# Performance work log

Measured on AMD Instinct MI355X. Metric: run time of the kernel, lower is better.

## Reference

```python
import jax, jax.numpy as jnp
import numpy as np

T_IN, T_TGT, B = 192, 192, 128
XDIM, CH, H, Z, OUT = 64, 2, 512, 128, 64
XIN = XDIM * CH


def _gru_cell(h, x_proj, Whh, bhh):
    # torch GRU gate order: r, z, n
    hp = h @ Whh.T + bhh
    xr, xz, xn = jnp.split(x_proj, 3, axis=-1)
    hr, hz, hn = jnp.split(hp, 3, axis=-1)
    r = jax.nn.sigmoid(xr + hr)
    zg = jax.nn.sigmoid(xz + hz)
    n = jnp.tanh(xn + r * hn)
    return (1.0 - zg) * n + zg * h


def _run_gru(xs, h0, Wih, bih, Whh, bhh):
    xp = xs @ Wih.T + bih  # [T, B, 3H] precomputed input projections
    def step(h, xpt):
        h2 = _gru_cell(h, xpt, Whh, bhh)
        return h2, h2
    hT, outs = jax.lax.scan(step, h0, xp)
    return outs, hT


def setup_inputs() -> dict:
    key = jax.random.key(0)
    ks = jax.random.split(key, 40)
    p = lambda i, shape: jax.random.normal(ks[i], shape, jnp.float32) * 0.05
    inp = {
        "x": jax.random.normal(ks[0], (T_IN, B, XIN), jnp.float32),
        "target": jax.random.normal(ks[1], (T_TGT, B, XDIM), jnp.float32),
        "eps_z": jax.random.normal(ks[2], (2, B, Z), jnp.float32),
        "eps_y": jax.random.normal(ks[3], (T_TGT, B, OUT), jnp.float32),
        # phi_x MLP
        "W_phi1": p(4, (H, XIN)), "b_phi1": jnp.zeros((H,), jnp.float32),
        "W_phi2": p(5, (H, H)), "b_phi2": jnp.zeros((H,), jnp.float32),
        # encoder bidirectional GRU
        "Wih_ef": p(6, (3 * H, H)), "bih_ef": jnp.zeros((3 * H,), jnp.float32),
        "Whh_ef": p(7, (3 * H, H)), "bhh_ef": jnp.zeros((3 * H,), jnp.float32),
        "Wih_eb": p(8, (3 * H, H)), "bih_eb": jnp.zeros((3 * H,), jnp.float32),
        "Whh_eb": p(9, (3 * H, H)), "bhh_eb": jnp.zeros((3 * H,), jnp.float32),
        # latent heads
        "W_mean": p(10, (Z, H)), "b_mean": jnp.zeros((Z,), jnp.float32),
        "W_std": p(11, (Z, H)), "b_std": jnp.zeros((Z,), jnp.float32),
        # first decoder hidden
        "W_fh": p(12, (H, 2 * Z)), "b_fh": jnp.zeros((H,), jnp.float32),
        # decoder GRU, input size H + 2Z (order: [z_expanded, state])
        "Wih_d": p(13, (3 * H, 2 * Z + H)), "bih_d": jnp.zeros((3 * H,), jnp.float32),
        "Whh_d": p(14, (3 * H, H)), "bhh_d": jnp.zeros((3 * H,), jnp.float32),
        # decoder output heads
        "W_dm": p(15, (OUT, H)), "b_dm": jnp.zeros((OUT,), jnp.float32),
        "W_ds": p(16, (OUT, H)), "b_ds": jnp.zeros((OUT,), jnp.float32),
        "epoch": 0,
    }
    return inp


def reference(x, target, eps_z, eps_y,
              W_phi1, b_phi1, W_phi2, b_phi2,
              Wih_ef, bih_ef, Whh_ef, bhh_ef,
              Wih_eb, bih_eb, Whh_eb, bhh_eb,
              W_mean, b_mean, W_std, b_std,
              W_fh, b_fh, Wih_d, bih_d, Whh_d, bhh_d,
              W_dm, b_dm, W_ds, b_ds, epoch):
    Bsz, h_dim = x.shape[1], W_phi1.shape[0]
    two_z = W_fh.shape[1]
    # phi_x
    phi = jax.nn.relu(jax.nn.relu(x @ W_phi1.T + b_phi1) @ W_phi2.T + b_phi2)
    h0 = jnp.zeros((Bsz, h_dim), phi.dtype)
    # bidirectional encoder: final hidden of each direction
    _, hf = _run_gru(phi, h0, Wih_ef, bih_ef, Whh_ef, bhh_ef)
    _, hb = _run_gru(phi[::-1], h0, Wih_eb, bih_eb, Whh_eb, bhh_eb)
    enc_h = jnp.stack([hf, hb])  # [2, B, H]
    latent_mean = enc_h @ W_mean.T + b_mean
    latent_std = jax.nn.softplus(enc_h @ W_std.T + b_std)
    z = eps_z * latent_std + latent_mean  # [2, B, Z]
    z_exp = jnp.concatenate([z[0], z[1]], axis=1)  # [B, 2Z]
    dec_h0 = jnp.tanh(z_exp @ W_fh.T + b_fh)
    # decoder input = concat([z_exp, state]); split Wih_d columns accordingly
    W_z, W_s = Wih_d[:, :two_z], Wih_d[:, two_z:]
    z_proj = z_exp @ W_z.T + bih_d  # constant part of input projection

    def step(carry, eps_t):
        h, s = carry  # s is previous decoder_out (zeros at t=0)
        xp = z_proj + s @ W_s.T
        h2 = _gru_cell(h, xp, Whh_d, bhh_d)
        m = jax.nn.softplus(h2 @ W_dm.T + b_dm)
        st = jax.nn.softplus(h2 @ W_ds.T + b_ds)
        pred = eps_t * st + m
        return (h2, h2), (pred, m, st)

    s0 = jnp.zeros_like(dec_h0)
    _, (preds, means, stds) = jax.lax.scan(step, (dec_h0, s0), eps_y)
    return latent_mean, latent_std, z, preds, means, stds
```

## Files before the change

### kernel.cpp

```cpp
#include <hip/hip_runtime.h>
#include <stdint.h>

typedef __attribute__((ext_vector_type(4))) float    f32x4;
typedef __attribute__((ext_vector_type(8))) short    s16x8;
typedef __attribute__((ext_vector_type(4))) short    s16x4;
typedef __attribute__((ext_vector_type(4))) unsigned u32x4;
typedef __attribute__((ext_vector_type(8))) __bf16   bf16x8;

#define DEV __device__ __forceinline__

DEV float b2f(short h) {
  unsigned u = ((unsigned)(unsigned short)h) << 16;
  return __builtin_bit_cast(float, u);
}
DEV short f2b(float f) {
  unsigned u = __builtin_bit_cast(unsigned, f);
  u = (u + 0x7FFFu + ((u >> 16) & 1u)) >> 16;
  return (short)u;
}
DEV float fsig(float x) { return 1.0f / (1.0f + __expf(-x)); }
DEV float ftanh(float x) {
  x = fminf(fmaxf(x, -15.0f), 15.0f);
  float e = __expf(2.0f * x);
  return (e - 1.0f) / (e + 1.0f);
}
DEV float fsp(float x) { return (x > 20.0f) ? x : __logf(1.0f + __expf(x)); }

DEV f32x4 MFMA(s16x8 a, s16x8 b, f32x4 c) {
  return __builtin_amdgcn_mfma_f32_16x16x32_bf16(
      __builtin_bit_cast(bf16x8, a), __builtin_bit_cast(bf16x8, b), c, 0, 0, 0);
}
DEV void gload16(const void* g, void* l) {
  __builtin_amdgcn_global_load_lds(
      (const __attribute__((address_space(1))) unsigned*)g,
      (__attribute__((address_space(3))) unsigned*)l, 16, 0, 0);
}

DEV s16x8 ld16c(const short* p) {
  s16x8 r;
  asm volatile("global_load_dwordx4 %0, %1, off sc0 sc1" : "=v"(r) : "v"(p) : "memory");
  return r;
}
DEV void st8c(short* p, s16x4 v) {
  asm volatile("global_store_dwordx2 %0, %1, off sc0 sc1" :: "v"(p), "v"(v) : "memory");
}
DEV void stflagc(unsigned* p, unsigned v) {
  asm volatile("global_store_dword %0, %1, off sc0 sc1" :: "v"(p), "v"(v) : "memory");
}
DEV void poll8c(const unsigned* f, unsigned tgt) {
  unsigned gd = 0;
  for (;;) {
    u32x4 a, b;
    asm volatile("global_load_dwordx4 %0, %2, off sc0 sc1\n\t"
                 "global_load_dwordx4 %1, %2, off offset:16 sc0 sc1\n\t"
                 "s_waitcnt vmcnt(0)"
                 : "=v"(a), "=v"(b) : "v"(f) : "memory");
    unsigned m = a[0];
    m = a[1] < m ? a[1] : m; m = a[2] < m ? a[2] : m; m = a[3] < m ? a[3] : m;
    m = b[0] < m ? b[0] : m; m = b[1] < m ? b[1] : m;
    m = b[2] < m ? b[2] : m; m = b[3] < m ? b[3] : m;
    if (m >= tgt) return;
    if (++gd > (1u << 18)) return;
  }
}

__global__ void k_initf(unsigned* __restrict__ f) {
  stflagc(f + threadIdx.x * 2, 0u);
  stflagc(f + threadIdx.x * 2 + 1, 0u);
}
__global__ void k_inith(short* __restrict__ hBe, short* __restrict__ hBd) {
  int i = blockIdx.x * 256 + threadIdx.x;
  s16x4 v; v[0] = 1; v[1] = 1; v[2] = 1; v[3] = 1;
  if (i < 32768) {
    st8c(hBe + (size_t)i * 8, v);
    st8c(hBe + (size_t)i * 8 + 4, v);
  } else if (i < 49152) {
    int j = i - 32768;
    st8c(hBd + (size_t)j * 8, v);
    st8c(hBd + (size_t)j * 8 + 4, v);
  }
}

__global__ void k_f2b(const float* __restrict__ s, short* __restrict__ d, int n) {
  int i = (blockIdx.x * 256 + threadIdx.x) * 4;
  if (i >= n) return;
  float4 v = *(const float4*)(s + i);
  s16x4 o; o[0] = f2b(v.x); o[1] = f2b(v.y); o[2] = f2b(v.z); o[3] = f2b(v.w);
  *(s16x4*)(d + i) = o;
}
__global__ void k_f2bs(const float* __restrict__ s, short* __restrict__ d,
                       int cols, int sstr, int soff, int total) {
  int i = (blockIdx.x * 256 + threadIdx.x) * 4;
  if (i >= total) return;
  int r = i / cols, c = i - r * cols;
  float4 v = *(const float4*)(s + (size_t)r * sstr + soff + c);
  s16x4 o; o[0] = f2b(v.x); o[1] = f2b(v.y); o[2] = f2b(v.z); o[3] = f2b(v.w);
  *(s16x4*)(d + i) = o;
}
__global__ void k_build_dec(const float* __restrict__ Whh, const float* __restrict__ Wih,
                            short* __restrict__ out) {
  int i = (blockIdx.x * 256 + threadIdx.x) * 4;
  if (i >= 1048576) return;
  int r = i >> 9, c = i & 511;
  float4 v;
  if (r < 1024) {
    float4 a = *(const float4*)(Whh + (size_t)r * 512 + c);
    float4 b = *(const float4*)(Wih + (size_t)r * 768 + 256 + c);
    v = make_float4(a.x + b.x, a.y + b.y, a.z + b.z, a.w + b.w);
  } else if (r < 1536) {
    v = *(const float4*)(Wih + (size_t)r * 768 + 256 + c);
  } else {
    v = *(const float4*)(Whh + (size_t)(r - 512) * 512 + c);
  }
  s16x4 o; o[0] = f2b(v.x); o[1] = f2b(v.y); o[2] = f2b(v.z); o[3] = f2b(v.w);
  *(s16x4*)(out + i) = o;
}

template <int EPI>
__global__ __launch_bounds__(256) void kgemm(
    const short* __restrict__ A, const short* __restrict__ W,
    const float* __restrict__ bias, float* __restrict__ outF,
    short* __restrict__ outB, int M, int N, int K) {
  __shared__ short lA[8192];
  __shared__ short lB[8192];
  const int tid = threadIdx.x, lane = tid & 63, wid = tid >> 6;
  const int l15 = lane & 15, lq = lane >> 4;
  const int m0 = blockIdx.x * 128, n0 = blockIdx.y * 128;
  const int wr2 = wid >> 1, wc2 = wid & 1;
  const f32x4 vz = {0.f, 0.f, 0.f, 0.f};
  f32x4 acc[4][4];
#pragma unroll
  for (int i = 0; i < 4; ++i)
#pragma unroll
    for (int j = 0; j < 4; ++j) acc[i][j] = vz;
  const int Kb = K * 2;
  const int nkt = K >> 6;
  const int srow = lane >> 3, sk = (lane & 7) * 16;
  const char* gA = (const char*)A;
  const char* gW = (const char*)W;
  for (int kt = 0; kt < nkt; ++kt) {
    __syncthreads();
#pragma unroll
    for (int i = 0; i < 4; ++i) {
      const int c = wid * 4 + i;
      gload16(gA + (size_t)(m0 + c * 8 + srow) * Kb + kt * 128 + sk, (char*)lA + c * 1024);
      gload16(gW + (size_t)(n0 + c * 8 + srow) * Kb + kt * 128 + sk, (char*)lB + c * 1024);
    }
    __syncthreads();
#pragma unroll
    for (int kc = 0; kc < 2; ++kc) {
      s16x8 af[4], bf[4];
#pragma unroll
      for (int mt = 0; mt < 4; ++mt)
        af[mt] = *(const s16x8*)((const char*)lA + (wr2 * 64 + mt * 16 + l15) * 128 + kc * 64 + lq * 16);
#pragma unroll
      for (int nt = 0; nt < 4; ++nt)
        bf[nt] = *(const s16x8*)((const char*)lB + (wc2 * 64 + nt * 16 + l15) * 128 + kc * 64 + lq * 16);
#pragma unroll
      for (int mt = 0; mt < 4; ++mt)
#pragma unroll
        for (int nt = 0; nt < 4; ++nt)
          acc[mt][nt] = MFMA(af[mt], bf[nt], acc[mt][nt]);
    }
  }
#pragma unroll
  for (int mt = 0; mt < 4; ++mt) {
#pragma unroll
    for (int nt = 0; nt < 4; ++nt) {
      const int col = n0 + wc2 * 64 + nt * 16 + l15;
      const int rl = wr2 * 64 + mt * 16 + lq * 4;
      const int row = m0 + rl;
      const float bv = bias ? bias[col] : 0.f;
      if (EPI == 0) {
#pragma unroll
        for (int d = 0; d < 4; ++d) outF[(size_t)(row + d) * N + col] = acc[mt][nt][d] + bv;
      } else if (EPI == 1) {
#pragma unroll
        for (int d = 0; d < 4; ++d) {
          float v = acc[mt][nt][d] + bv;
          v = v > 0.f ? v : 0.f;
          outB[(size_t)(row + d) * N + col] = f2b(v);
        }
      } else if (EPI == 3) {
#pragma unroll
        for (int d = 0; d < 4; ++d) {
          float v = ftanh(acc[mt][nt][d] + bv);
          outF[(size_t)(row + d) * N + col] = v;
          outB[(size_t)(row + d) * N + col] = f2b(v);
        }
      } else {
#pragma unroll
        for (int d = 0; d < 4; ++d)
          outB[(size_t)(row + d) * N + col] = f2b(acc[mt][nt][d] + bv);
      }
    }
  }
}

DEV void enc_xp_load(const short* xp, int tt, int J0, int lq, int b,
                     short xv[3][4]) {
  const short* xr = xp + (size_t)(tt * 128 + b) * 1536;
#pragma unroll
  for (int g = 0; g < 3; ++g)
#pragma unroll
    for (int d = 0; d < 4; ++d)
      xv[g][d] = xr[g * 512 + J0 + lq * 4 + d];
}

__global__ __launch_bounds__(256, 1) void enc_scan(
    const short* __restrict__ xpTf, const short* __restrict__ xpTb,
    const short* __restrict__ Whf, const short* __restrict__ Whb,
    const float* __restrict__ bhf, const float* __restrict__ bhb,
    short* __restrict__ hB, short* __restrict__ ench,
    unsigned* __restrict__ flags) {
  const int tid = threadIdx.x, lane = tid & 63, wid = tid >> 6;
  const int l15 = lane & 15, lq = lane >> 4;
  const int w = blockIdx.x;
  const int gru = w >> 6, rr = w & 63, bg = rr >> 3, cw = rr & 7;
  const int J0 = (cw * 4 + wid) * 16, b0 = bg * 16;
  const int b = b0 + l15;
  const short* Wg = gru ? Whb : Whf;
  const float* bb = gru ? bhb : bhf;
  const short* xpT = gru ? xpTb : xpTf;
  short* hBg = hB + (size_t)gru * 131072;
  unsigned* gfl = flags + (gru * 8 + bg) * 16;
  const f32x4 vz = {0.f, 0.f, 0.f, 0.f};

  s16x8 wfr[3][16];
#pragma unroll
  for (int g = 0; g < 3; ++g) {
    const short* wrp = Wg + (size_t)(g * 512 + J0 + l15) * 512 + lq * 8;
#pragma unroll
    for (int kc = 0; kc < 16; ++kc) wfr[g][kc] = *(const s16x8*)(wrp + kc * 32);
  }
  float bi[3][4];
#pragma unroll
  for (int g = 0; g < 3; ++g)
#pragma unroll
    for (int d = 0; d < 4; ++d) bi[g][d] = bb[g * 512 + J0 + lq * 4 + d];
  float hpv[4];
#pragma unroll
  for (int d = 0; d < 4; ++d) hpv[d] = 0.f;

  short xpv[3][4];
  enc_xp_load(xpT, gru ? 191 : 0, J0, lq, b, xpv);
  const int chb = J0 + lq * 4;

  {
    s16x4 pk;
#pragma unroll
    for (int d = 0; d < 4; ++d) {
      float rg = fsig(b2f(xpv[0][d]) + bi[0][d]);
      float zg = fsig(b2f(xpv[1][d]) + bi[1][d]);
      float nn = ftanh(b2f(xpv[2][d]) + rg * bi[2][d]);
      float hv = (1.f - zg) * nn;
      hpv[d] = hv;
      pk[d] = f2b(hv);
    }
    pk[0] = (short)(pk[0] & ~1);
    st8c(hBg + (((size_t)((chb >> 3) * 128 + b)) << 3) + (chb & 7), pk);
    asm volatile("s_waitcnt vmcnt(0)" ::: "memory");
    __syncthreads();
    if (tid == 0) stflagc(gfl + cw, 1u);
    enc_xp_load(xpT, gru ? 190 : 1, J0, lq, b, xpv);
  }

  for (int t = 1; t < 192; ++t) {
    const int E = ((t - 1) >> 1) & 1;
    const int T = (t >> 1) & 1;
    const short* hsrc = hBg + ((t + 1) & 1) * 65536;
    s16x8 hb[16];
    bool fresh = false;
    for (int it = 0; it < 24; ++it) {
#pragma unroll
      for (int kc = 0; kc < 16; ++kc)
        hb[kc] = ld16c(hsrc + ((size_t)((kc * 4 + lq) * 128 + b) << 3));
      asm volatile("s_waitcnt vmcnt(0)" ::: "memory");
      unsigned ok = 1u;
#pragma unroll
      for (int kc = 0; kc < 16; ++kc)
        ok &= (unsigned)((hb[kc][0] & 1) == E) & (unsigned)((hb[kc][4] & 1) == E);
      if (__all((int)ok)) { fresh = true; break; }
    }
    if (!fresh) {
      poll8c(gfl, (unsigned)t);
#pragma unroll
      for (int kc = 0; kc < 16; ++kc)
        hb[kc] = ld16c(hsrc + ((size_t)((kc * 4 + lq) * 128 + b) << 3));
      asm volatile("s_waitcnt vmcnt(0)" ::: "memory");
    }
    __builtin_amdgcn_sched_barrier(0);
    f32x4 acc[3];
#pragma unroll
    for (int g = 0; g < 3; ++g) acc[g] = vz;
#pragma unroll
    for (int kc = 0; kc < 16; ++kc)
#pragma unroll
      for (int g = 0; g < 3; ++g) acc[g] = MFMA(wfr[g][kc], hb[kc], acc[g]);
    short* hdst = hBg + (t & 1) * 65536;
    s16x4 pk;
#pragma unroll
    for (int d = 0; d < 4; ++d) {
      float rg = fsig(b2f(xpv[0][d]) + acc[0][d] + bi[0][d]);
      float zg = fsig(b2f(xpv[1][d]) + acc[1][d] + bi[1][d]);
      float nn = ftanh(b2f(xpv[2][d]) + rg * (acc[2][d] + bi[2][d]));
      float hv = (1.f - zg) * nn + zg * hpv[d];
      hpv[d] = hv;
      pk[d] = f2b(hv);
    }
    pk[0] = (short)((pk[0] & ~1) | T);
    st8c(hdst + (((size_t)((chb >> 3) * 128 + b)) << 3) + (chb & 7), pk);
    if (t == 191) *(s16x4*)(ench + (size_t)gru * 65536 + (size_t)b * 512 + chb) = pk;
    asm volatile("s_waitcnt vmcnt(0)" ::: "memory");
    __syncthreads();
    if (tid == 0) stflagc(gfl + cw, (unsigned)(t + 1));
    if (t < 191) {
      const int tp = t + 1;
      enc_xp_load(xpT, gru ? (191 - tp) : tp, J0, lq, b, xpv);
    }
  }
}

__global__ __launch_bounds__(256, 1) void dec_scan(
    const short* __restrict__ zpR, const short* __restrict__ Wd,
    const float* __restrict__ bhd, const float* __restrict__ pre0,
    const float* __restrict__ h0f, short* __restrict__ hB,
    short* __restrict__ Hs, unsigned* __restrict__ flags) {
  const int tid = threadIdx.x, lane = tid & 63, wid = tid >> 6;
  const int l15 = lane & 15, lq = lane >> 4;
  const int w = blockIdx.x;
  const int bg = w >> 3, m = w & 7;
  unsigned* gfl = flags + 256 + bg * 16;
  const int J0 = (m * 4 + wid) * 16, b0 = bg * 16;
  const int b = b0 + l15;
  const f32x4 vz = {0.f, 0.f, 0.f, 0.f};

  s16x8 wfr[4][16];
#pragma unroll
  for (int g = 0; g < 4; ++g) {
    const short* wrp = Wd + (size_t)(g * 512 + J0 + l15) * 512 + lq * 8;
#pragma unroll
    for (int kc = 0; kc < 16; ++kc) wfr[g][kc] = *(const s16x8*)(wrp + kc * 32);
  }
  float bi[3][4];
#pragma unroll
  for (int g = 0; g < 3; ++g)
#pragma unroll
    for (int d = 0; d < 4; ++d) bi[g][d] = bhd[g * 512 + J0 + lq * 4 + d];
  short zpv[3][4];
#pragma unroll
  for (int g = 0; g < 3; ++g)
#pragma unroll
    for (int d = 0; d < 4; ++d)
      zpv[g][d] = zpR[(size_t)b * 1536 + g * 512 + J0 + lq * 4 + d];
  float hpv[4];
#pragma unroll
  for (int d = 0; d < 4; ++d) hpv[d] = h0f[(size_t)b * 512 + J0 + lq * 4 + d];
  const int chb = J0 + lq * 4;

  {
    s16x4 pk;
#pragma unroll
    for (int d = 0; d < 4; ++d) {
      float p0 = pre0[(size_t)b * 1536 + 0 * 512 + J0 + lq * 4 + d];
      float p1 = pre0[(size_t)b * 1536 + 1 * 512 + J0 + lq * 4 + d];
      float p2 = pre0[(size_t)b * 1536 + 2 * 512 + J0 + lq * 4 + d];
      float rg = fsig(b2f(zpv[0][d]) + p0);
      float zg = fsig(b2f(zpv[1][d]) + p1);
      float nn = ftanh(b2f(zpv[2][d]) + rg * p2);
      float hv = (1.f - zg) * nn + zg * hpv[d];
      hpv[d] = hv;
      pk[d] = f2b(hv);
    }
    pk[0] = (short)(pk[0] & ~1);
    st8c(hB + (((size_t)((chb >> 3) * 128 + b)) << 3) + (chb & 7), pk);
    asm volatile("s_waitcnt vmcnt(0)" ::: "memory");
    __syncthreads();
    if (tid == 0) stflagc(gfl + m, 1u);
    *(s16x4*)(Hs + (size_t)b * 512 + chb) = pk;
  }

  for (int t = 1; t < 192; ++t) {
    const int E = ((t - 1) >> 1) & 1;
    const int T = (t >> 1) & 1;
    const short* hsrc = hB + ((t + 1) & 1) * 65536;
    s16x8 hb[16];
    bool fresh = false;
    for (int it = 0; it < 24; ++it) {
#pragma unroll
      for (int kc = 0; kc < 16; ++kc)
        hb[kc] = ld16c(hsrc + ((size_t)((kc * 4 + lq) * 128 + b) << 3));
      asm volatile("s_waitcnt vmcnt(0)" ::: "memory");
      unsigned ok = 1u;
#pragma unroll
      for (int kc = 0; kc < 16; ++kc)
        ok &= (unsigned)((hb[kc][0] & 1) == E) & (unsigned)((hb[kc][4] & 1) == E);
      if (__all((int)ok)) { fresh = true; break; }
    }
    if (!fresh) {
      poll8c(gfl, (unsigned)t);
#pragma unroll
      for (int kc = 0; kc < 16; ++kc)
        hb[kc] = ld16c(hsrc + ((size_t)((kc * 4 + lq) * 128 + b) << 3));
      asm volatile("s_waitcnt vmcnt(0)" ::: "memory");
    }
    __builtin_amdgcn_sched_barrier(0);
    f32x4 acc[4];
#pragma unroll
    for (int g = 0; g < 4; ++g) acc[g] = vz;
#pragma unroll
    for (int kc = 0; kc < 16; ++kc)
#pragma unroll
      for (int g = 0; g < 4; ++g) acc[g] = MFMA(wfr[g][kc], hb[kc], acc[g]);
    short* hdst = hB + (t & 1) * 65536;
    s16x4 pk;
#pragma unroll
    for (int d = 0; d < 4; ++d) {
      float rg = fsig(b2f(zpv[0][d]) + acc[0][d] + bi[0][d]);
      float zg = fsig(b2f(zpv[1][d]) + acc[1][d] + bi[1][d]);
      float nn = ftanh(b2f(zpv[2][d]) + acc[2][d] + rg * (acc[3][d] + bi[2][d]));
      float hv = (1.f - zg) * nn + zg * hpv[d];
      hpv[d] = hv;
      pk[d] = f2b(hv);
    }
    pk[0] = (short)((pk[0] & ~1) | T);
    st8c(hdst + (((size_t)((chb >> 3) * 128 + b)) << 3) + (chb & 7), pk);
    asm volatile("s_waitcnt vmcnt(0)" ::: "memory");
    __syncthreads();
    if (tid == 0) stflagc(gfl + m, (unsigned)(t + 1));
    *(s16x4*)(Hs + (size_t)(t * 128 + b) * 512 + chb) = pk;
  }
}

__global__ void k_latent(const float* __restrict__ tmp, const float* __restrict__ b_mean,
                         const float* __restrict__ b_std, const float* __restrict__ eps_z,
                         float* __restrict__ out, short* __restrict__ zexp) {
  int i = blockIdx.x * 256 + threadIdx.x;
  if (i >= 32768) return;
  int c = i & 127, b = (i >> 7) & 127, g = i >> 14;
  float mp = tmp[(size_t)(g * 128 + b) * 256 + c] + b_mean[c];
  float sp = fsp(tmp[(size_t)(g * 128 + b) * 256 + 128 + c] + b_std[c]);
  float zv = eps_z[i] * sp + mp;
  out[i] = mp;
  out[32768 + i] = sp;
  out[65536 + i] = zv;
  zexp[b * 256 + g * 128 + c] = f2b(zv);
}

__global__ void k_preds(const float* __restrict__ tmp2, const float* __restrict__ b_dm,
                        const float* __restrict__ b_ds, const float* __restrict__ eps_y,
                        float* __restrict__ out) {
  int j = blockIdx.x * 256 + threadIdx.x;
  if (j >= 1572864) return;
  int c = j & 63;
  int row = j >> 6;
  float m = fsp(tmp2[(size_t)row * 128 + c] + b_dm[c]);
  float st = fsp(tmp2[(size_t)row * 128 + 64 + c] + b_ds[c]);
  out[98304 + j] = eps_y[j] * st + m;
  out[1671168 + j] = m;
  out[3244032 + j] = st;
}

extern "C" void kernel_launch(void* const* d_in, const int* in_sizes, int n_in,
                              void* d_out, int out_size, void* d_ws, size_t ws_size,
                              hipStream_t stream) {
  (void)in_sizes; (void)n_in; (void)out_size; (void)ws_size;
  const float* x      = (const float*)d_in[0];
  const float* eps_z  = (const float*)d_in[2];
  const float* eps_y  = (const float*)d_in[3];
  const float* W_phi1 = (const float*)d_in[4];
  const float* b_phi1 = (const float*)d_in[5];
  const float* W_phi2 = (const float*)d_in[6];
  const float* b_phi2 = (const float*)d_in[7];
  const float* Wih_ef = (const float*)d_in[8];
  const float* bih_ef = (const float*)d_in[9];
  const float* Whh_ef = (const float*)d_in[10];
  const float* bhh_ef = (const float*)d_in[11];
  const float* Wih_eb = (const float*)d_in[12];
  const float* bih_eb = (const float*)d_in[13];
  const float* Whh_eb = (const float*)d_in[14];
  const float* bhh_eb = (const float*)d_in[15];
  const float* W_mean = (const float*)d_in[16];
  const float* b_mean = (const float*)d_in[17];
  const float* W_std  = (const float*)d_in[18];
  const float* b_std  = (const float*)d_in[19];
  const float* W_fh   = (const float*)d_in[20];
  const float* b_fh   = (const float*)d_in[21];
  const float* Wih_d  = (const float*)d_in[22];
  const float* bih_d  = (const float*)d_in[23];
  const float* Whh_d  = (const float*)d_in[24];
  const float* bhh_d  = (const float*)d_in[25];
  const float* W_dm   = (const float*)d_in[26];
  const float* b_dm   = (const float*)d_in[27];
  const float* W_ds   = (const float*)d_in[28];
  const float* b_ds   = (const float*)d_in[29];
  float* out = (float*)d_out;
  char* ws = (char*)d_ws;

  short* x16  = (short*)(ws + 0);
  short* C1   = (short*)(ws + 6291456);
  short* Hs   = (short*)(ws + 0);
  short* phi  = (short*)(ws + 31457280);
  float* tmp2 = (float*)(ws + 31457280);
  short* xpf  = (short*)(ws + 56623104);
  short* xpb  = (short*)(ws + 132120576);
  short* w_dec = (short*)(ws + 56623104);
  float* pre0F = (float*)(ws + 58720256);
  short* h0b   = (short*)(ws + 59506688);
  char*  wb   = ws + 207618048;
  short* w_phi1_16 = (short*)(wb + 0);
  short* w_phi2_16 = (short*)(wb + 131072);
  short* w_ihef = (short*)(wb + 655360);
  short* w_hhef = (short*)(wb + 2228224);
  short* w_iheb = (short*)(wb + 3801088);
  short* w_hheb = (short*)(wb + 5373952);
  short* w_ms   = (short*)(wb + 6946816);
  short* w_fh   = (short*)(wb + 7208960);
  short* w_z    = (short*)(wb + 7471104);
  short* w_hhd  = (short*)(wb + 9830400);
  short* w_out  = (short*)(wb + 11403264);
  short* hBe   = (short*)(ws + 219152384);
  short* ench  = (short*)(ws + 219676672);
  float* tmpms = (float*)(ws + 219938816);
  short* zexp  = (short*)(ws + 220200960);
  float* h0f   = (float*)(ws + 220266496);
  short* hBd   = (short*)(ws + 220528640);
  short* zpR   = (short*)(ws + 220790784);
  unsigned* flags  = (unsigned*)(ws + 221184000);

  k_initf<<<1, 256, 0, stream>>>(flags);
  k_inith<<<192, 256, 0, stream>>>(hBe, hBd);

  k_f2b<<<3072, 256, 0, stream>>>(x, x16, 3145728);
  k_f2b<<<64,   256, 0, stream>>>(W_phi1, w_phi1_16, 65536);
  k_f2b<<<256,  256, 0, stream>>>(W_phi2, w_phi2_16, 262144);
  k_f2b<<<768,  256, 0, stream>>>(Wih_ef, w_ihef, 786432);
  k_f2b<<<768,  256, 0, stream>>>(Whh_ef, w_hhef, 786432);
  k_f2b<<<768,  256, 0, stream>>>(Wih_eb, w_iheb, 786432);
  k_f2b<<<768,  256, 0, stream>>>(Whh_eb, w_hheb, 786432);
  k_f2b<<<64,   256, 0, stream>>>(W_mean, w_ms, 65536);
  k_f2b<<<64,   256, 0, stream>>>(W_std,  w_ms + 65536, 65536);
  k_f2b<<<128,  256, 0, stream>>>(W_fh, w_fh, 131072);
  k_f2b<<<768,  256, 0, stream>>>(Whh_d, w_hhd, 786432);
  k_f2b<<<32,   256, 0, stream>>>(W_dm, w_out, 32768);
  k_f2b<<<32,   256, 0, stream>>>(W_ds, w_out + 32768, 32768);
  k_f2bs<<<384, 256, 0, stream>>>(Wih_d, w_z, 256, 768, 0, 393216);

  kgemm<1><<<dim3(192, 4), 256, 0, stream>>>(x16, w_phi1_16, b_phi1, (float*)nullptr, C1, 24576, 512, 128);
  kgemm<1><<<dim3(192, 4), 256, 0, stream>>>(C1, w_phi2_16, b_phi2, (float*)nullptr, phi, 24576, 512, 512);
  kgemm<4><<<dim3(192, 12), 256, 0, stream>>>(phi, w_ihef, bih_ef, (float*)nullptr, xpf, 24576, 1536, 512);
  kgemm<4><<<dim3(192, 12), 256, 0, stream>>>(phi, w_iheb, bih_eb, (float*)nullptr, xpb, 24576, 1536, 512);
  enc_scan<<<128, 256, 0, stream>>>(xpf, xpb, w_hhef, w_hheb, bhh_ef, bhh_eb, hBe, ench, flags);
  k_build_dec<<<1024, 256, 0, stream>>>(Whh_d, Wih_d, w_dec);
  kgemm<0><<<dim3(2, 2), 256, 0, stream>>>(ench, w_ms, (const float*)nullptr, tmpms, (short*)nullptr, 256, 256, 512);
  k_latent<<<128, 256, 0, stream>>>(tmpms, b_mean, b_std, eps_z, out, zexp);
  kgemm<3><<<dim3(1, 4), 256, 0, stream>>>(zexp, w_fh, b_fh, h0f, h0b, 128, 512, 256);
  kgemm<4><<<dim3(1, 12), 256, 0, stream>>>(zexp, w_z, bih_d, (float*)nullptr, zpR, 128, 1536, 256);
  kgemm<0><<<dim3(1, 12), 256, 0, stream>>>(h0b, w_hhd, bhh_d, pre0F, (short*)nullptr, 128, 1536, 512);
  dec_scan<<<64, 256, 0, stream>>>(zpR, w_dec, bhh_d, pre0F, h0f, hBd, Hs, flags);
  kgemm<0><<<dim3(192, 1), 256, 0, stream>>>(Hs, w_out, (const float*)nullptr, tmp2, (short*)nullptr, 24576, 128, 512);
  k_preds<<<6144, 256, 0, stream>>>(tmp2, b_dm, b_ds, eps_y, out);
}
```

Measured before the change: 1.413 ms.

## Fuse encoder input projection into recurrent scan kernel

Drops the two large input-projection GEMMs for the encoder GRUs. The scan kernel instead keeps the input weights resident in registers and computes each step's input projection with MFMAs from phi before waiting on the hidden-state handoff. This removes the writing and reading of a large bf16 projection buffer and two kernel launches. In exchange the per-step work inside the serial scan grows, register pressure doubles (96 weight fragments per lane, which may spill), and the input projection bias is now added in fp32 instead of being pre-rounded to bf16.

Result: slower. 2.075 ms (+46.9%).

```diff
diff --git a/kernel.cpp b/kernel.cpp
--- a/kernel.cpp
+++ b/kernel.cpp
@@ -197,20 +197,12 @@
   }
 }
 
-DEV void enc_xp_load(const short* xp, int tt, int J0, int lq, int b,
-                     short xv[3][4]) {
-  const short* xr = xp + (size_t)(tt * 128 + b) * 1536;
-#pragma unroll
-  for (int g = 0; g < 3; ++g)
-#pragma unroll
-    for (int d = 0; d < 4; ++d)
-      xv[g][d] = xr[g * 512 + J0 + lq * 4 + d];
-}
-
 __global__ __launch_bounds__(256, 1) void enc_scan(
-    const short* __restrict__ xpTf, const short* __restrict__ xpTb,
+    const short* __restrict__ phi,
     const short* __restrict__ Whf, const short* __restrict__ Whb,
+    const short* __restrict__ Wif, const short* __restrict__ Wib,
     const float* __restrict__ bhf, const float* __restrict__ bhb,
+    const float* __restrict__ bif, const float* __restrict__ bib,
     short* __restrict__ hB, short* __restrict__ ench,
     unsigned* __restrict__ flags) {
   const int tid = threadIdx.x, lane = tid & 63, wid = tid >> 6;
@@ -220,39 +212,57 @@
   const int J0 = (cw * 4 + wid) * 16, b0 = bg * 16;
   const int b = b0 + l15;
   const short* Wg = gru ? Whb : Whf;
-  const float* bb = gru ? bhb : bhf;
-  const short* xpT = gru ? xpTb : xpTf;
+  const short* Wi = gru ? Wib : Wif;
+  const float* bbh = gru ? bhb : bhf;
+  const float* bbi = gru ? bib : bif;
   short* hBg = hB + (size_t)gru * 131072;
   unsigned* gfl = flags + (gru * 8 + bg) * 16;
   const f32x4 vz = {0.f, 0.f, 0.f, 0.f};
 
-  s16x8 wfr[3][16];
+  s16x8 wfh[3][16], wfi[3][16];
 #pragma unroll
   for (int g = 0; g < 3; ++g) {
     const short* wrp = Wg + (size_t)(g * 512 + J0 + l15) * 512 + lq * 8;
-#pragma unroll
-    for (int kc = 0; kc < 16; ++kc) wfr[g][kc] = *(const s16x8*)(wrp + kc * 32);
-  }
-  float bi[3][4];
+    const short* wip = Wi + (size_t)(g * 512 + J0 + l15) * 512 + lq * 8;
+#pragma unroll
+    for (int kc = 0; kc < 16; ++kc) {
+      wfh[g][kc] = *(const s16x8*)(wrp + kc * 32);
+      wfi[g][kc] = *(const s16x8*)(wip + kc * 32);
+    }
+  }
+  float bh[3][4], bi[3][4];
 #pragma unroll
   for (int g = 0; g < 3; ++g)
 #pragma unroll
-    for (int d = 0; d < 4; ++d) bi[g][d] = bb[g * 512 + J0 + lq * 4 + d];
+    for (int d = 0; d < 4; ++d) {
+      bh[g][d] = bbh[g * 512 + J0 + lq * 4 + d];
+      bi[g][d] = bbi[g * 512 + J0 + lq * 4 + d];
+    }
   float hpv[4];
 #pragma unroll
   for (int d = 0; d < 4; ++d) hpv[d] = 0.f;
 
-  short xpv[3][4];
-  enc_xp_load(xpT, gru ? 191 : 0, J0, lq, b, xpv);
   const int chb = J0 + lq * 4;
 
   {
+    const int tt = gru ? 191 : 0;
+    const short* pr = phi + (size_t)(tt * 128 + b) * 512 + lq * 8;
+    s16x8 phf[16];
+#pragma unroll
+    for (int kc = 0; kc < 16; ++kc) phf[kc] = *(const s16x8*)(pr + kc * 32);
+    f32x4 ai[3];
+#pragma unroll
+    for (int g = 0; g < 3; ++g) ai[g] = vz;
+#pragma unroll
+    for (int kc = 0; kc < 16; ++kc)
+#pragma unroll
+      for (int g = 0; g < 3; ++g) ai[g] = MFMA(wfi[g][kc], phf[kc], ai[g]);
     s16x4 pk;
 #pragma unroll
     for (int d = 0; d < 4; ++d) {
-      float rg = fsig(b2f(xpv[0][d]) + bi[0][d]);
-      float zg = fsig(b2f(xpv[1][d]) + bi[1][d]);
-      float nn = ftanh(b2f(xpv[2][d]) + rg * bi[2][d]);
+      float rg = fsig(ai[0][d] + bi[0][d] + bh[0][d]);
+      float zg = fsig(ai[1][d] + bi[1][d] + bh[1][d]);
+      float nn = ftanh(ai[2][d] + bi[2][d] + rg * bh[2][d]);
       float hv = (1.f - zg) * nn;
       hpv[d] = hv;
       pk[d] = f2b(hv);
@@ -262,13 +272,17 @@
     asm volatile("s_waitcnt vmcnt(0)" ::: "memory");
     __syncthreads();
     if (tid == 0) stflagc(gfl + cw, 1u);
-    enc_xp_load(xpT, gru ? 190 : 1, J0, lq, b, xpv);
   }
 
   for (int t = 1; t < 192; ++t) {
     const int E = ((t - 1) >> 1) & 1;
     const int T = (t >> 1) & 1;
     const short* hsrc = hBg + ((t + 1) & 1) * 65536;
+    const int tt = gru ? (191 - t) : t;
+    const short* pr = phi + (size_t)(tt * 128 + b) * 512 + lq * 8;
+    s16x8 phf[16];
+#pragma unroll
+    for (int kc = 0; kc < 16; ++kc) phf[kc] = *(const s16x8*)(pr + kc * 32);
     s16x8 hb[16];
     bool fresh = false;
     for (int it = 0; it < 24; ++it) {
@@ -290,20 +304,24 @@
       asm volatile("s_waitcnt vmcnt(0)" ::: "memory");
     }
     __builtin_amdgcn_sched_barrier(0);
-    f32x4 acc[3];
-#pragma unroll
-    for (int g = 0; g < 3; ++g) acc[g] = vz;
+    f32x4 ai[3], ah[3];
+#pragma unroll
+    for (int g = 0; g < 3; ++g) { ai[g] = vz; ah[g] = vz; }
 #pragma unroll
     for (int kc = 0; kc < 16; ++kc)
 #pragma unroll
-      for (int g = 0; g < 3; ++g) acc[g] = MFMA(wfr[g][kc], hb[kc], acc[g]);
+      for (int g = 0; g < 3; ++g) ai[g] = MFMA(wfi[g][kc], phf[kc], ai[g]);
+#pragma unroll
+    for (int kc = 0; kc < 16; ++kc)
+#pragma unroll
+      for (int g = 0; g < 3; ++g) ah[g] = MFMA(wfh[g][kc], hb[kc], ah[g]);
     short* hdst = hBg + (t & 1) * 65536;
     s16x4 pk;
 #pragma unroll
     for (int d = 0; d < 4; ++d) {
-      float rg = fsig(b2f(xpv[0][d]) + acc[0][d] + bi[0][d]);
-      float zg = fsig(b2f(xpv[1][d]) + acc[1][d] + bi[1][d]);
-      float nn = ftanh(b2f(xpv[2][d]) + rg * (acc[2][d] + bi[2][d]));
+      float rg = fsig(ai[0][d] + bi[0][d] + ah[0][d] + bh[0][d]);
+      float zg = fsig(ai[1][d] + bi[1][d] + ah[1][d] + bh[1][d]);
+      float nn = ftanh(ai[2][d] + bi[2][d] + rg * (ah[2][d] + bh[2][d]));
       float hv = (1.f - zg) * nn + zg * hpv[d];
       hpv[d] = hv;
       pk[d] = f2b(hv);
@@ -314,10 +332,6 @@
     asm volatile("s_waitcnt vmcnt(0)" ::: "memory");
     __syncthreads();
     if (tid == 0) stflagc(gfl + cw, (unsigned)(t + 1));
-    if (t < 191) {
-      const int tp = t + 1;
-      enc_xp_load(xpT, gru ? (191 - tp) : tp, J0, lq, b, xpv);
-    }
   }
 }
 
@@ -502,8 +516,6 @@
   short* Hs   = (short*)(ws + 0);
   short* phi  = (short*)(ws + 31457280);
   float* tmp2 = (float*)(ws + 31457280);
-  short* xpf  = (short*)(ws + 56623104);
-  short* xpb  = (short*)(ws + 132120576);
   short* w_dec = (short*)(ws + 56623104);
   float* pre0F = (float*)(ws + 58720256);
   short* h0b   = (short*)(ws + 59506688);
@@ -548,9 +560,8 @@
 
   kgemm<1><<<dim3(192, 4), 256, 0, stream>>>(x16, w_phi1_16, b_phi1, (float*)nullptr, C1, 24576, 512, 128);
   kgemm<1><<<dim3(192, 4), 256, 0, stream>>>(C1, w_phi2_16, b_phi2, (float*)nullptr, phi, 24576, 512, 512);
-  kgemm<4><<<dim3(192, 12), 256, 0, stream>>>(phi, w_ihef, bih_ef, (float*)nullptr, xpf, 24576, 1536, 512);
-  kgemm<4><<<dim3(192, 12), 256, 0, stream>>>(phi, w_iheb, bih_eb, (float*)nullptr, xpb, 24576, 1536, 512);
-  enc_scan<<<128, 256, 0, stream>>>(xpf, xpb, w_hhef, w_hheb, bhh_ef, bhh_eb, hBe, ench, flags);
+  enc_scan<<<128, 256, 0, stream>>>(phi, w_hhef, w_hheb, w_ihef, w_iheb,
+                                    bhh_ef, bhh_eb, bih_ef, bih_eb, hBe, ench, flags);
   k_build_dec<<<1024, 256, 0, stream>>>(Whh_d, Wih_d, w_dec);
   kgemm<0><<<dim3(2, 2), 256, 0, stream>>>(ench, w_ms, (const float*)nullptr, tmpms, (short*)nullptr, 256, 256, 512);
   k_latent<<<128, 256, 0, stream>>>(tmpms, b_mean, b_std, eps_z, out, zexp);
```
